# Optimization experiments

Measured on AMD Instinct MI355X. Metric: run time of the kernel, lower is better.

Reference implementation:

```python
import jax, jax.numpy as jnp
import numpy as np

N, E, T = 50000, 200000, 100000
D, H, C = 512, 512, 7
BN_EPS = 1e-5


def _bn(h, g, b):
    # BatchNorm1d with batch statistics (training-mode stats, biased var as torch)
    m = jnp.mean(h, axis=0)
    v = jnp.var(h, axis=0)
    return (h - m) * jax.lax.rsqrt(v + BN_EPS) * g + b


def _forward(x, graph, edge_index, train_edge_id,
             W_sub, bn1_g, bn1_b, fcx_W, fcx_b, eps1,
             g_W1, g_b1, g_W2, g_b2, gbn_g, gbn_b,
             lin1_W, lin1_b, lin2_W, lin2_b, fc2_W, fc2_b):
    src, dst = edge_index[0], edge_index[1]
    n = x.shape[0]

    # SubgraphGNNKernel approximation: one GINConv (eps=0), mlp_layers=1 linear
    # (bias=False per bias=False), residual add (res=True)
    agg_s = graph + jax.ops.segment_sum(graph[src], dst, num_segments=n)
    sub_x = agg_s @ W_sub + graph  # [N, D]
    sub_x = jax.nn.relu(_bn(sub_x, bn1_g, bn1_b))  # dropout: eval no-op

    # fc_x
    h = x @ fcx_W + fcx_b  # [N, D]

    # GINConv: mlp((1+eps)*h + sum_{j->i} h_j)
    agg = (1.0 + eps1) * h + jax.ops.segment_sum(h[src], dst, num_segments=n)
    h = jax.nn.relu(agg @ g_W1 + g_b1)
    h = jax.nn.relu(h @ g_W2 + g_b2)
    h = _bn(h, gbn_g, gbn_b)  # [N, H]

    # lin1 -> relu -> (dropout eval no-op) -> lin2, add subgraph branch
    h = jax.nn.relu(h @ lin1_W + lin1_b)
    h = h @ lin2_W + lin2_b
    h = h + sub_x  # [N, H]

    # link prediction: gather endpoints of training edges, elementwise mul
    nid = edge_index[:, train_edge_id]  # [2, T]
    pair = h[nid[0]] * h[nid[1]]  # [T, H]
    return pair @ fc2_W + fc2_b  # [T, C]


def setup_inputs() -> dict:
    key = jax.random.key(0)
    ks = jax.random.split(key, 20)
    w = lambda k, shape: (jax.random.normal(k, shape, jnp.float32)
                          * (1.0 / np.sqrt(shape[0])))
    return {
        "x": jax.random.normal(ks[0], (N, D), jnp.float32),
        "graph": jax.random.normal(ks[1], (N, D), jnp.float32),
        "edge_index": jax.random.randint(ks[2], (2, E), 0, N),
        "train_edge_id": jax.random.randint(ks[3], (T,), 0, E),
        "W_sub": w(ks[4], (D, D)),
        "bn1_g": jnp.ones((D,), jnp.float32),
        "bn1_b": jnp.zeros((D,), jnp.float32),
        "fcx_W": w(ks[5], (D, D)),
        "fcx_b": jnp.zeros((D,), jnp.float32),
        "eps1": jnp.zeros((), jnp.float32),
        "g_W1": w(ks[6], (D, H)),
        "g_b1": jnp.zeros((H,), jnp.float32),
        "g_W2": w(ks[7], (H, H)),
        "g_b2": jnp.zeros((H,), jnp.float32),
        "gbn_g": jnp.ones((H,), jnp.float32),
        "gbn_b": jnp.zeros((H,), jnp.float32),
        "lin1_W": w(ks[8], (H, H)),
        "lin1_b": jnp.zeros((H,), jnp.float32),
        "lin2_W": w(ks[9], (H, H)),
        "lin2_b": jnp.zeros((H,), jnp.float32),
        "fc2_W": w(ks[10], (H, C)),
        "fc2_b": jnp.zeros((C,), jnp.float32),
    }


def reference(x, graph, edge_index, train_edge_id,
              W_sub, bn1_g, bn1_b, fcx_W, fcx_b, eps1,
              g_W1, g_b1, g_W2, g_b2, gbn_g, gbn_b,
              lin1_W, lin1_b, lin2_W, lin2_b, fc2_W, fc2_b):
    return _forward(x, graph, edge_index, train_edge_id,
                    W_sub, bn1_g, bn1_b, fcx_W, fcx_b, eps1,
                    g_W1, g_b1, g_W2, g_b2, gbn_g, gbn_b,
                    lin1_W, lin1_b, lin2_W, lin2_b, fc2_W, fc2_b)
```

## Files before the change

kernel.cpp:

```cpp
#include <hip/hip_runtime.h>

#define N_NODES 50000
#define N_EDGES 200000
#define N_TRAIN 100000
#define DIM     512
#define NCLS    7
#define NSB     ((N_NODES + 255) / 256)

typedef unsigned short ushort;
typedef _Float16 f16x8 __attribute__((ext_vector_type(8)));
typedef float    f32x4 __attribute__((ext_vector_type(4)));

__device__ __forceinline__ ushort f2h(float f) {
    _Float16 h = (_Float16)f;
    union { _Float16 h; ushort u; } v; v.h = h; return v.u;
}

__device__ __forceinline__ void gload_lds16(const void* g, void* l) {
    __builtin_amdgcn_global_load_lds((const __attribute__((address_space(1))) unsigned int*)g,
                                     (__attribute__((address_space(3))) unsigned int*)l,
                                     16, 0, 0);
}

#define VMWAIT(N) asm volatile("s_waitcnt vmcnt(" #N ")" ::: "memory")
#define LGKM0()   asm volatile("s_waitcnt lgkmcnt(0)" ::: "memory")
#define BAR() do { asm volatile("" ::: "memory"); __builtin_amdgcn_s_barrier(); \
                   asm volatile("" ::: "memory"); } while (0)


__global__ void zero_kernel(float* p, int n) {
    int i = blockIdx.x * blockDim.x + threadIdx.x;
    if (i < n) p[i] = 0.0f;
}


__global__ void hist_kernel(const int* __restrict__ ei, int* __restrict__ cnt) {
    int e = blockIdx.x * blockDim.x + threadIdx.x;
    if (e < N_EDGES) atomicAdd(&cnt[ei[N_EDGES + e]], 1);
}

__global__ __launch_bounds__(256) void scan1_kernel(const int* __restrict__ cnt,
                                                    int* __restrict__ off,
                                                    int* __restrict__ bsum) {
    __shared__ int s[256];
    int t = threadIdx.x, b = blockIdx.x;
    int i = b * 256 + t;
    s[t] = (i < N_NODES) ? cnt[i] : 0;
    __syncthreads();
    for (int d = 1; d < 256; d <<= 1) {
        int add = (t >= d) ? s[t - d] : 0;
        __syncthreads();
        s[t] += add;
        __syncthreads();
    }
    if (i < N_NODES) off[i + 1] = s[t];
    if (t == 255) bsum[b] = s[255];
}

__global__ __launch_bounds__(256) void scan2_kernel(int* bsum) {
    __shared__ int s[256];
    int t = threadIdx.x;
    s[t] = (t < NSB) ? bsum[t] : 0;
    __syncthreads();
    for (int d = 1; d < 256; d <<= 1) {
        int add = (t >= d) ? s[t - d] : 0;
        __syncthreads();
        s[t] += add;
        __syncthreads();
    }
    if (t < NSB) bsum[t] = s[t];
}

__global__ __launch_bounds__(256) void scan3_kernel(int* off, const int* __restrict__ bsum) {
    int t = threadIdx.x, b = blockIdx.x;
    int i = b * 256 + t;
    if (i == 0) off[0] = 0;
    if (i < N_NODES) off[i + 1] += (b > 0 ? bsum[b - 1] : 0);
}

__global__ void fillprep_kernel(const int* __restrict__ off, int* __restrict__ wcur) {
    int i = blockIdx.x * blockDim.x + threadIdx.x;
    if (i < N_NODES) wcur[i] = off[i];
}

__global__ void fill_kernel(const int* __restrict__ ei, int* __restrict__ wcur,
                            int* __restrict__ srclist) {
    int e = blockIdx.x * blockDim.x + threadIdx.x;
    if (e < N_EDGES) {
        int d = ei[N_EDGES + e];
        int pos = atomicAdd(&wcur[d], 1);
        srclist[pos] = ei[e];
    }
}


__global__ __launch_bounds__(128) void gather_h_kernel(const float* __restrict__ feat,
                                                       const float* __restrict__ base,
                                                       const float* eps_or_null,
                                                       const int* __restrict__ off,
                                                       const int* __restrict__ srclist,
                                                       ushort* __restrict__ oh) {
    int n = blockIdx.x;
    int t = threadIdx.x;
    float s = 1.0f;
    if (eps_or_null) s = 1.0f + *eps_or_null;
    int e0 = off[n], e1 = off[n + 1];
    float4 acc = ((const float4*)(base + (size_t)n * DIM))[t];
    acc.x *= s; acc.y *= s; acc.z *= s; acc.w *= s;
    for (int e = e0; e < e1; ++e) {
        int srcn = srclist[e];
        float4 v = ((const float4*)(feat + (size_t)srcn * DIM))[t];
        acc.x += v.x; acc.y += v.y; acc.z += v.z; acc.w += v.w;
    }
    size_t o = (size_t)n * DIM + t * 4;
    ushort4 r;
    r.x = f2h(acc.x); r.y = f2h(acc.y); r.z = f2h(acc.z); r.w = f2h(acc.w);
    *(ushort4*)(oh + o) = r;
}

__global__ void convert_h_kernel(const float* __restrict__ X,
                                 ushort* __restrict__ oh, size_t n4) {
    size_t i = (size_t)blockIdx.x * blockDim.x + threadIdx.x;
    size_t stride = (size_t)gridDim.x * blockDim.x;
    const float4* X4 = (const float4*)X;
    for (; i < n4; i += stride) {
        float4 v = X4[i];
        ushort4 r;
        r.x = f2h(v.x); r.y = f2h(v.y); r.z = f2h(v.z); r.w = f2h(v.w);
        *(ushort4*)(oh + i * 4) = r;
    }
}

__global__ void wconvert6_kernel(const float* __restrict__ W0, const float* __restrict__ W1,
                                 const float* __restrict__ W2, const float* __restrict__ W3,
                                 const float* __restrict__ W4, const float* __restrict__ W5,
                                 ushort* __restrict__ wt) {
    int p = blockIdx.y;
    const float* W = (p == 0) ? W0 : (p == 1) ? W1 : (p == 2) ? W2
                   : (p == 3) ? W3 : (p == 4) ? W4 : W5;
    ushort* Th = wt + (size_t)p * 262144;
    int idx = blockIdx.x * 256 + threadIdx.x;
    int n = idx >> 9, k = idx & 511;
    Th[idx] = f2h(W[k * DIM + n]);
}


__global__ __launch_bounds__(512, 6) void gemm_f16_kernel(
    const ushort* __restrict__ Ahp,
    const ushort* __restrict__ Wf,
    const float* __restrict__ bias,
    const float* __restrict__ addmat,
    const float* __restrict__ bnst,
    float* __restrict__ Cf,
    ushort* __restrict__ Oh,
    float* __restrict__ stats,
    int M, int relu, int mode)
{
    __shared__ __align__(16) char smem[3 * 16384];

    int tid = threadIdx.x;
    int w = tid >> 6;
    int l = tid & 63;
    int wm = w >> 2;
    int wn = w & 3;

    int nwg = gridDim.x;
    int q = nwg >> 3, r = nwg & 7;
    int xcd = blockIdx.x & 7, idx = blockIdx.x >> 3;
    int wgid = (xcd < r ? xcd * (q + 1) : r * (q + 1) + (xcd - r) * q) + idx;
    int bm = (wgid >> 2) * 128;
    int bn = (wgid & 3) * 128;

    f32x4 acc[4][2];
#pragma unroll
    for (int i = 0; i < 4; i++)
#pragma unroll
        for (int j = 0; j < 2; j++) acc[i][j] = (f32x4){0.f, 0.f, 0.f, 0.f};

    int ro = l & 15;
    int co = l >> 4;

    size_t soff[2]; int lofs[2];
#pragma unroll
    for (int t2 = 0; t2 < 2; t2++) {
        int c = 2 * w + t2;
        int row0, base_; bool cl;
        if (c < 8) { row0 = c * 16;       base_ = bm; cl = true;  lofs[t2] = c * 1024; }
        else       { row0 = (c - 8) * 16; base_ = bn; cl = false; lofs[t2] = 8192 + (c - 8) * 1024; }
        int lrit = row0 + (l >> 2);
        int rr = base_ + lrit;
        if (cl) rr = min(rr, M - 1);
        int kc = (l & 3) ^ ((lrit >> 1) & 3);
        soff[t2] = (size_t)rr * DIM + kc * 8;
    }
    const ushort* sp0 = (2 * w < 8) ? Ahp : Wf;
    const ushort* sp1 = (2 * w + 1 < 8) ? Ahp : Wf;

    int aoff[4], woff[2];
#pragma unroll
    for (int i = 0; i < 4; i++) {
        int arow = wm * 64 + i * 16 + ro;
        aoff[i] = arow * 64 + ((co ^ ((arow >> 1) & 3)) << 4);
    }
#pragma unroll
    for (int j = 0; j < 2; j++) {
        int wrow = wn * 32 + j * 16 + ro;
        woff[j] = 8192 + wrow * 64 + ((co ^ ((wrow >> 1) & 3)) << 4);
    }

#define STAGE(BB, K0) do {                                                        \
    char* sb_ = smem + (BB) * 16384;                                              \
    gload_lds16(sp0 + soff[0] + (K0), sb_ + lofs[0]);                             \
    gload_lds16(sp1 + soff[1] + (K0), sb_ + lofs[1]);                             \
} while (0)

#define COMPUTE(BB) do {                                                          \
    const char* bb_ = (const char*)smem + (BB) * 16384;                           \
    f16x8 fa[4], fw2[2];                                                          \
    _Pragma("unroll")                                                             \
    for (int i = 0; i < 4; i++) fa[i] = *(const f16x8*)(bb_ + aoff[i]);           \
    _Pragma("unroll")                                                             \
    for (int j = 0; j < 2; j++) fw2[j] = *(const f16x8*)(bb_ + woff[j]);          \
    __builtin_amdgcn_s_setprio(1);                                                \
    _Pragma("unroll")                                                             \
    for (int i = 0; i < 4; i++)                                                   \
        _Pragma("unroll")                                                         \
        for (int j = 0; j < 2; j++)                                               \
            acc[i][j] = __builtin_amdgcn_mfma_f32_16x16x32_f16(fa[i], fw2[j], acc[i][j], 0, 0, 0); \
    __builtin_amdgcn_s_setprio(0);                                                \
} while (0)

    STAGE(0, 0);
    STAGE(1, 32);
    STAGE(2, 64);

    int bufi = 0;
    for (int ks = 0; ks < 16; ks++) {
        if (ks < 14)      { VMWAIT(4); }
        else if (ks == 14){ VMWAIT(2); }
        else              { VMWAIT(0); }
        BAR();
        COMPUTE(bufi);
        LGKM0();
        BAR();
        if (ks <= 12) STAGE(bufi, (ks + 3) * 32);
        bufi = (bufi == 2) ? 0 : bufi + 1;
    }

#undef STAGE
#undef COMPUTE

    int colbase = bn + wn * 32 + ro;
    int rowbase = bm + wm * 64 + co * 4;
    float sacc[2] = {0.f, 0.f};
    float qacc[2] = {0.f, 0.f};
#pragma unroll
    for (int j = 0; j < 2; j++) {
        int col = colbase + j * 16;
        float bi = bias ? bias[col] : 0.f;
        float sc = 0.f, sh = 0.f;
        if (bnst) { sc = bnst[1024 + col]; sh = bnst[1536 + col]; }
#pragma unroll
        for (int i = 0; i < 4; i++) {
#pragma unroll
            for (int rg = 0; rg < 4; rg++) {
                int row = rowbase + i * 16 + rg;
                if (row < M) {
                    float v = acc[i][j][rg] + bi;
                    if (addmat) {
                        float am = addmat[(size_t)row * DIM + col];
                        if (bnst) am = fmaxf(am * sc + sh, 0.f);
                        v += am;
                    }
                    if (relu) v = fmaxf(v, 0.f);
                    if (mode == 0) Cf[(size_t)row * DIM + col] = v;
                    else           Oh[(size_t)row * DIM + col] = f2h(v);
                    if (stats) { sacc[j] += v; qacc[j] += v * v; }
                }
            }
        }
    }
    if (stats) {
#pragma unroll
        for (int j = 0; j < 2; j++) {
            float ss = sacc[j], qq = qacc[j];
            ss += __shfl_xor(ss, 16); qq += __shfl_xor(qq, 16);
            ss += __shfl_xor(ss, 32); qq += __shfl_xor(qq, 32);
            if (co == 0) {
                int col = colbase + j * 16;
                atomicAdd(&stats[col], ss);
                atomicAdd(&stats[DIM + col], qq);
            }
        }
    }
}


__global__ void bn_finalize_kernel(float* st, const float* __restrict__ g,
                                   const float* __restrict__ b, int M) {
    int c = threadIdx.x;
    float mean = st[c] / (float)M;
    float var = st[DIM + c] / (float)M - mean * mean;
    float sc = g[c] * rsqrtf(var + 1e-5f);
    st[1024 + c] = sc;
    st[1536 + c] = b[c] - mean * sc;
}

__global__ void bn_apply_kernel(const float* __restrict__ X, const float* __restrict__ st,
                                float* __restrict__ Yf, ushort* __restrict__ Yh,
                                int M, int relu, int mode) {
    const float* scale = st + 1024;
    const float* shift = st + 1536;
    size_t n4 = (size_t)M * DIM / 4;
    size_t i = (size_t)blockIdx.x * blockDim.x + threadIdx.x;
    size_t stride = (size_t)gridDim.x * blockDim.x;
    const float4* X4 = (const float4*)X;
    for (; i < n4; i += stride) {
        int col4 = (int)(i & (DIM / 4 - 1)) * 4;
        float4 v = X4[i];
        v.x = v.x * scale[col4 + 0] + shift[col4 + 0];
        v.y = v.y * scale[col4 + 1] + shift[col4 + 1];
        v.z = v.z * scale[col4 + 2] + shift[col4 + 2];
        v.w = v.w * scale[col4 + 3] + shift[col4 + 3];
        if (relu) {
            v.x = fmaxf(v.x, 0.f); v.y = fmaxf(v.y, 0.f);
            v.z = fmaxf(v.z, 0.f); v.w = fmaxf(v.w, 0.f);
        }
        if (mode == 0) {
            ((float4*)Yf)[i] = v;
        } else {
            ushort4 rr;
            rr.x = f2h(v.x); rr.y = f2h(v.y); rr.z = f2h(v.z); rr.w = f2h(v.w);
            *(ushort4*)(Yh + i * 4) = rr;
        }
    }
}


__global__ __launch_bounds__(256) void pair_kernel(const float* __restrict__ H,
                                                   const int* __restrict__ ei,
                                                   const int* __restrict__ teid,
                                                   const float* __restrict__ W,
                                                   const float* __restrict__ bias,
                                                   float* __restrict__ out) {
    int lane = threadIdx.x & 63;
    int wid = blockIdx.x * 4 + (threadIdx.x >> 6);
    int nw = gridDim.x * 4;
    int d0 = lane * 8;

    float wreg[8][NCLS];
#pragma unroll
    for (int qd = 0; qd < 8; qd++)
#pragma unroll
        for (int c = 0; c < NCLS; c++)
            wreg[qd][c] = W[(d0 + qd) * NCLS + c];
    float bi[NCLS];
#pragma unroll
    for (int c = 0; c < NCLS; c++) bi[c] = bias[c];

    for (int t = wid; t < N_TRAIN; t += nw) {
        int id = teid[t];
        int n0 = ei[id];
        int n1 = ei[N_EDGES + id];
        const float4* a4 = (const float4*)(H + (size_t)n0 * DIM);
        const float4* b4 = (const float4*)(H + (size_t)n1 * DIM);
        float4 a0 = a4[lane * 2], a1 = a4[lane * 2 + 1];
        float4 b0 = b4[lane * 2], b1 = b4[lane * 2 + 1];
        float p[8] = {a0.x * b0.x, a0.y * b0.y, a0.z * b0.z, a0.w * b0.w,
                      a1.x * b1.x, a1.y * b1.y, a1.z * b1.z, a1.w * b1.w};
        float acc[NCLS];
#pragma unroll
        for (int c = 0; c < NCLS; c++) acc[c] = 0.f;
#pragma unroll
        for (int qd = 0; qd < 8; qd++)
#pragma unroll
            for (int c = 0; c < NCLS; c++) acc[c] += p[qd] * wreg[qd][c];
#pragma unroll
        for (int off = 32; off; off >>= 1)
#pragma unroll
            for (int c = 0; c < NCLS; c++) acc[c] += __shfl_down(acc[c], off);
        if (lane == 0) {
#pragma unroll
            for (int c = 0; c < NCLS; c++) out[(size_t)t * NCLS + c] = acc[c] + bi[c];
        }
    }
}


extern "C" void kernel_launch(void* const* d_in, const int* in_sizes, int n_in,
                              void* d_out, int out_size, void* d_ws, size_t ws_size,
                              hipStream_t stream) {
    const float* x      = (const float*)d_in[0];
    const float* graph  = (const float*)d_in[1];
    const int*   ei     = (const int*)d_in[2];
    const int*   teid   = (const int*)d_in[3];
    const float* W_sub  = (const float*)d_in[4];
    const float* bn1_g  = (const float*)d_in[5];
    const float* bn1_b  = (const float*)d_in[6];
    const float* fcx_W  = (const float*)d_in[7];
    const float* fcx_b  = (const float*)d_in[8];
    const float* eps1   = (const float*)d_in[9];
    const float* g_W1   = (const float*)d_in[10];
    const float* g_b1   = (const float*)d_in[11];
    const float* g_W2   = (const float*)d_in[12];
    const float* g_b2   = (const float*)d_in[13];
    const float* gbn_g  = (const float*)d_in[14];
    const float* gbn_b  = (const float*)d_in[15];
    const float* lin1_W = (const float*)d_in[16];
    const float* lin1_b = (const float*)d_in[17];
    const float* lin2_W = (const float*)d_in[18];
    const float* lin2_b = (const float*)d_in[19];
    const float* fc2_W  = (const float*)d_in[20];
    const float* fc2_b  = (const float*)d_in[21];
    float* out = (float*)d_out;

    char* ws = (char*)d_ws;
    size_t NB = (size_t)N_NODES * DIM * sizeof(float);
    float* slotA = (float*)(ws);
    float* slotB = (float*)(ws + NB);
    float* slotC = (float*)(ws + 2 * NB);
    float* st1   = (float*)(ws + 3 * NB);
    float* st2   = st1 + 2048;
    int* off     = (int*)(st2 + 2048);
    int* wcur    = off + (N_NODES + 1);
    int* srclist = wcur + N_NODES;
    int* bsum    = srclist + N_EDGES;
    ushort* wt   = (ushort*)(bsum + 256);
    ushort* Wsub_f = wt;
    ushort* fcx_f  = wt + 1 * 262144;
    ushort* gw1_f  = wt + 2 * 262144;
    ushort* gw2_f  = wt + 3 * 262144;
    ushort* lw1_f  = wt + 4 * 262144;
    ushort* lw2_f  = wt + 5 * 262144;

    ushort* A_h = (ushort*)slotA;
    ushort* C_h = (ushort*)slotC;

    size_t n4 = (size_t)N_NODES * DIM / 4;
    int mt = (N_NODES + 127) / 128;
    dim3 ggrid(mt * 4);

    zero_kernel<<<16, 256, 0, stream>>>(st1, 4096);
    zero_kernel<<<NSB, 256, 0, stream>>>((float*)wcur, N_NODES);

    hist_kernel<<<(N_EDGES + 255) / 256, 256, 0, stream>>>(ei, wcur);
    scan1_kernel<<<NSB, 256, 0, stream>>>(wcur, off, bsum);
    scan2_kernel<<<1, 256, 0, stream>>>(bsum);
    scan3_kernel<<<NSB, 256, 0, stream>>>(off, bsum);
    fillprep_kernel<<<NSB, 256, 0, stream>>>(off, wcur);
    fill_kernel<<<(N_EDGES + 255) / 256, 256, 0, stream>>>(ei, wcur, srclist);

    wconvert6_kernel<<<dim3(1024, 6), 256, 0, stream>>>(W_sub, fcx_W, g_W1, g_W2, lin1_W, lin2_W, wt);

    gather_h_kernel<<<N_NODES, 128, 0, stream>>>(graph, graph, nullptr, off, srclist, A_h);
    gemm_f16_kernel<<<ggrid, 512, 0, stream>>>(A_h, Wsub_f, nullptr, graph, nullptr,
                                               slotB, nullptr, st1, N_NODES, 0, 0);
    bn_finalize_kernel<<<1, 512, 0, stream>>>(st1, bn1_g, bn1_b, N_NODES);

    convert_h_kernel<<<2048, 256, 0, stream>>>(x, A_h, n4);
    gemm_f16_kernel<<<ggrid, 512, 0, stream>>>(A_h, fcx_f, fcx_b, nullptr, nullptr,
                                               slotC, nullptr, nullptr, N_NODES, 0, 0);

    gather_h_kernel<<<N_NODES, 128, 0, stream>>>(slotC, slotC, eps1, off, srclist, A_h);

    gemm_f16_kernel<<<ggrid, 512, 0, stream>>>(A_h, gw1_f, g_b1, nullptr, nullptr,
                                               nullptr, C_h, nullptr, N_NODES, 1, 1);
    gemm_f16_kernel<<<ggrid, 512, 0, stream>>>(C_h, gw2_f, g_b2, nullptr, nullptr,
                                               slotA, nullptr, st2, N_NODES, 1, 0);
    bn_finalize_kernel<<<1, 512, 0, stream>>>(st2, gbn_g, gbn_b, N_NODES);
    bn_apply_kernel<<<2048, 256, 0, stream>>>(slotA, st2, nullptr, C_h, N_NODES, 0, 1);

    gemm_f16_kernel<<<ggrid, 512, 0, stream>>>(C_h, lw1_f, lin1_b, nullptr, nullptr,
                                               nullptr, A_h, nullptr, N_NODES, 1, 1);
    gemm_f16_kernel<<<ggrid, 512, 0, stream>>>(A_h, lw2_f, lin2_b, slotB, st1,
                                               slotC, nullptr, nullptr, N_NODES, 0, 0);

    pair_kernel<<<2048, 256, 0, stream>>>(slotC, ei, teid, fc2_W, fc2_b, out);
}
```

Before: 783.3 us.

## Fold GIN BatchNorm into lin1 weights and keep intermediates in fp16

The BatchNorm after the GIN MLP is folded algebraically into lin1: the weights are scaled per input row by the BN scale and the BN shift is pushed into a new bias, which removes the separate bn_apply pass. Intermediate activations (sub_x pre-BN, fc_x output, the GIN MLP output) are now stored as fp16 instead of fp32, and a new fp16 gather kernel reads half the bytes per neighbor. The cost is two small folding kernels per call and extra fp16 rounding on values that feed statistics and residuals, which may affect accuracy.

Measured after the change: 731.6 us. -6.6%, faster.

```diff
diff --git a/kernel.cpp b/kernel.cpp
--- a/kernel.cpp
+++ b/kernel.cpp
@@ -14,6 +14,9 @@
 __device__ __forceinline__ ushort f2h(float f) {
     _Float16 h = (_Float16)f;
     union { _Float16 h; ushort u; } v; v.h = h; return v.u;
+}
+__device__ __forceinline__ float h2f(ushort u) {
+    union { ushort u; _Float16 h; } v; v.u = u; return (float)v.h;
 }
 
 __device__ __forceinline__ void gload_lds16(const void* g, void* l) {
@@ -118,6 +121,33 @@
     *(ushort4*)(oh + o) = r;
 }
 
+
+__global__ __launch_bounds__(128) void gather_h16_kernel(const ushort* __restrict__ feat,
+                                                         const ushort* __restrict__ base,
+                                                         const float* eps_or_null,
+                                                         const int* __restrict__ off,
+                                                         const int* __restrict__ srclist,
+                                                         ushort* __restrict__ oh) {
+    int n = blockIdx.x;
+    int t = threadIdx.x;
+    float s = 1.0f;
+    if (eps_or_null) s = 1.0f + *eps_or_null;
+    int e0 = off[n], e1 = off[n + 1];
+    ushort4 b4 = ((const ushort4*)(base + (size_t)n * DIM))[t];
+    float4 acc;
+    acc.x = h2f(b4.x) * s; acc.y = h2f(b4.y) * s;
+    acc.z = h2f(b4.z) * s; acc.w = h2f(b4.w) * s;
+    for (int e = e0; e < e1; ++e) {
+        int srcn = srclist[e];
+        ushort4 v = ((const ushort4*)(feat + (size_t)srcn * DIM))[t];
+        acc.x += h2f(v.x); acc.y += h2f(v.y); acc.z += h2f(v.z); acc.w += h2f(v.w);
+    }
+    size_t o = (size_t)n * DIM + t * 4;
+    ushort4 r;
+    r.x = f2h(acc.x); r.y = f2h(acc.y); r.z = f2h(acc.z); r.w = f2h(acc.w);
+    *(ushort4*)(oh + o) = r;
+}
+
 __global__ void convert_h_kernel(const float* __restrict__ X,
                                  ushort* __restrict__ oh, size_t n4) {
     size_t i = (size_t)blockIdx.x * blockDim.x + threadIdx.x;
@@ -144,12 +174,29 @@
     Th[idx] = f2h(W[k * DIM + n]);
 }
 
+__global__ void wfold_kernel(const float* __restrict__ W1, const float* __restrict__ st2,
+                             ushort* __restrict__ lw1s) {
+    int idx = blockIdx.x * 256 + threadIdx.x;
+    int n = idx >> 9, k = idx & 511;
+    lw1s[idx] = f2h(W1[k * DIM + n] * st2[1024 + k]);
+}
+
+__global__ void bfold_kernel(const float* __restrict__ W1, const float* __restrict__ b1,
+                             const float* __restrict__ st2, float* __restrict__ b1f) {
+    int c = threadIdx.x;
+    float s = 0.f;
+#pragma unroll 8
+    for (int k = 0; k < DIM; k++) s += st2[1536 + k] * W1[k * DIM + c];
+    b1f[c] = b1[c] + s;
+}
+
 
 __global__ __launch_bounds__(512, 6) void gemm_f16_kernel(
     const ushort* __restrict__ Ahp,
     const ushort* __restrict__ Wf,
     const float* __restrict__ bias,
-    const float* __restrict__ addmat,
+    const float* __restrict__ addmat_f,
+    const ushort* __restrict__ addmat_h,
     const float* __restrict__ bnst,
     float* __restrict__ Cf,
     ushort* __restrict__ Oh,
@@ -267,8 +314,9 @@
                 int row = rowbase + i * 16 + rg;
                 if (row < M) {
                     float v = acc[i][j][rg] + bi;
-                    if (addmat) {
-                        float am = addmat[(size_t)row * DIM + col];
+                    if (addmat_f || addmat_h) {
+                        float am = addmat_f ? addmat_f[(size_t)row * DIM + col]
+                                            : h2f(addmat_h[(size_t)row * DIM + col]);
                         if (bnst) am = fmaxf(am * sc + sh, 0.f);
                         v += am;
                     }
@@ -304,36 +352,6 @@
     float sc = g[c] * rsqrtf(var + 1e-5f);
     st[1024 + c] = sc;
     st[1536 + c] = b[c] - mean * sc;
-}
-
-__global__ void bn_apply_kernel(const float* __restrict__ X, const float* __restrict__ st,
-                                float* __restrict__ Yf, ushort* __restrict__ Yh,
-                                int M, int relu, int mode) {
-    const float* scale = st + 1024;
-    const float* shift = st + 1536;
-    size_t n4 = (size_t)M * DIM / 4;
-    size_t i = (size_t)blockIdx.x * blockDim.x + threadIdx.x;
-    size_t stride = (size_t)gridDim.x * blockDim.x;
-    const float4* X4 = (const float4*)X;
-    for (; i < n4; i += stride) {
-        int col4 = (int)(i & (DIM / 4 - 1)) * 4;
-        float4 v = X4[i];
-        v.x = v.x * scale[col4 + 0] + shift[col4 + 0];
-        v.y = v.y * scale[col4 + 1] + shift[col4 + 1];
-        v.z = v.z * scale[col4 + 2] + shift[col4 + 2];
-        v.w = v.w * scale[col4 + 3] + shift[col4 + 3];
-        if (relu) {
-            v.x = fmaxf(v.x, 0.f); v.y = fmaxf(v.y, 0.f);
-            v.z = fmaxf(v.z, 0.f); v.w = fmaxf(v.w, 0.f);
-        }
-        if (mode == 0) {
-            ((float4*)Yf)[i] = v;
-        } else {
-            ushort4 rr;
-            rr.x = f2h(v.x); rr.y = f2h(v.y); rr.z = f2h(v.z); rr.w = f2h(v.w);
-            *(ushort4*)(Yh + i * 4) = rr;
-        }
-    }
 }
 
 
@@ -432,11 +450,15 @@
     ushort* gw2_f  = wt + 3 * 262144;
     ushort* lw1_f  = wt + 4 * 262144;
     ushort* lw2_f  = wt + 5 * 262144;
-
-    ushort* A_h = (ushort*)slotA;
-    ushort* C_h = (ushort*)slotC;
-
-    size_t n4 = (size_t)N_NODES * DIM / 4;
+    ushort* lw1s   = wt + 6 * 262144;
+    float*  b1f    = (float*)(lw1s + 262144);
+
+    size_t HN = (size_t)N_NODES * DIM;
+    ushort* A_h  = (ushort*)slotA;       ushort* A2_h = A_h + HN;
+    ushort* B_h  = (ushort*)slotB;       ushort* B2_h = B_h + HN;
+    ushort* C2_h = (ushort*)slotC;
+
+    size_t n4 = HN / 4;
     int mt = (N_NODES + 127) / 128;
     dim3 ggrid(mt * 4);
 
@@ -453,27 +475,29 @@
     wconvert6_kernel<<<dim3(1024, 6), 256, 0, stream>>>(W_sub, fcx_W, g_W1, g_W2, lin1_W, lin2_W, wt);
 
     gather_h_kernel<<<N_NODES, 128, 0, stream>>>(graph, graph, nullptr, off, srclist, A_h);
-    gemm_f16_kernel<<<ggrid, 512, 0, stream>>>(A_h, Wsub_f, nullptr, graph, nullptr,
-                                               slotB, nullptr, st1, N_NODES, 0, 0);
+    gemm_f16_kernel<<<ggrid, 512, 0, stream>>>(A_h, Wsub_f, nullptr, graph, nullptr, nullptr,
+                                               nullptr, B_h, st1, N_NODES, 0, 1);
     bn_finalize_kernel<<<1, 512, 0, stream>>>(st1, bn1_g, bn1_b, N_NODES);
 
     convert_h_kernel<<<2048, 256, 0, stream>>>(x, A_h, n4);
-    gemm_f16_kernel<<<ggrid, 512, 0, stream>>>(A_h, fcx_f, fcx_b, nullptr, nullptr,
+    gemm_f16_kernel<<<ggrid, 512, 0, stream>>>(A_h, fcx_f, fcx_b, nullptr, nullptr, nullptr,
+                                               nullptr, C2_h, nullptr, N_NODES, 0, 1);
+
+    gather_h16_kernel<<<N_NODES, 128, 0, stream>>>(C2_h, C2_h, eps1, off, srclist, A_h);
+
+    gemm_f16_kernel<<<ggrid, 512, 0, stream>>>(A_h, gw1_f, g_b1, nullptr, nullptr, nullptr,
+                                               nullptr, B2_h, nullptr, N_NODES, 1, 1);
+    gemm_f16_kernel<<<ggrid, 512, 0, stream>>>(B2_h, gw2_f, g_b2, nullptr, nullptr, nullptr,
+                                               nullptr, A2_h, st2, N_NODES, 1, 1);
+    bn_finalize_kernel<<<1, 512, 0, stream>>>(st2, gbn_g, gbn_b, N_NODES);
+
+    wfold_kernel<<<1024, 256, 0, stream>>>(lin1_W, st2, lw1s);
+    bfold_kernel<<<1, 512, 0, stream>>>(lin1_W, lin1_b, st2, b1f);
+
+    gemm_f16_kernel<<<ggrid, 512, 0, stream>>>(A2_h, lw1s, b1f, nullptr, nullptr, nullptr,
+                                               nullptr, A_h, nullptr, N_NODES, 1, 1);
+    gemm_f16_kernel<<<ggrid, 512, 0, stream>>>(A_h, lw2_f, lin2_b, nullptr, B_h, st1,
                                                slotC, nullptr, nullptr, N_NODES, 0, 0);
 
-    gather_h_kernel<<<N_NODES, 128, 0, stream>>>(slotC, slotC, eps1, off, srclist, A_h);
-
-    gemm_f16_kernel<<<ggrid, 512, 0, stream>>>(A_h, gw1_f, g_b1, nullptr, nullptr,
-                                               nullptr, C_h, nullptr, N_NODES, 1, 1);
-    gemm_f16_kernel<<<ggrid, 512, 0, stream>>>(C_h, gw2_f, g_b2, nullptr, nullptr,
-                                               slotA, nullptr, st2, N_NODES, 1, 0);
-    bn_finalize_kernel<<<1, 512, 0, stream>>>(st2, gbn_g, gbn_b, N_NODES);
-    bn_apply_kernel<<<2048, 256, 0, stream>>>(slotA, st2, nullptr, C_h, N_NODES, 0, 1);
-
-    gemm_f16_kernel<<<ggrid, 512, 0, stream>>>(C_h, lw1_f, lin1_b, nullptr, nullptr,
-                                               nullptr, A_h, nullptr, N_NODES, 1, 1);
-    gemm_f16_kernel<<<ggrid, 512, 0, stream>>>(A_h, lw2_f, lin2_b, slotB, st1,
-                                               slotC, nullptr, nullptr, N_NODES, 0, 0);
-
     pair_kernel<<<2048, 256, 0, stream>>>(slotC, ei, teid, fc2_W, fc2_b, out);
 }
```
